# Performance work log

Hardware: AMD Instinct MI355X
Metric: run time of the kernel (lower is better)

The kernel has to match this reference:

```python
import jax, jax.numpy as jnp
import numpy as np

B, N, D, H = 32, 4096, 768, 384

def setup_inputs() -> dict:
    key = jax.random.key(0)
    k1, k2, k3 = jax.random.split(key, 3)
    patch_tokens = jax.random.normal(k1, (B, N, D), dtype=jnp.float32)
    # score head params (kaiming-like scale)
    w1 = jax.random.normal(k2, (D, H), dtype=jnp.float32) * (2.0 / H) ** 0.5
    b1 = jnp.zeros((H,), dtype=jnp.float32)
    w2 = jax.random.normal(k3, (H,), dtype=jnp.float32) * (2.0 / 1) ** 0.5
    b2 = jnp.zeros((), dtype=jnp.float32)
    return {"patch_tokens": patch_tokens, "w1": w1, "b1": b1, "w2": w2, "b2": b2,
            "keep_ratio_pct": 50}

def reference(patch_tokens, w1, b1, w2, b2, keep_ratio_pct):
    # score head: Linear -> GELU (erf variant, torch default) -> Linear(->1)
    h = jax.nn.gelu(jnp.einsum('bnd,dh->bnh', patch_tokens, w1) + b1, approximate=False)
    patch_logits = jnp.einsum('bnh,h->bn', h, w2) + b2                 # [B, N]
    foreground_scores = jax.nn.sigmoid(patch_logits)                    # [B, N]

    patch_count = patch_tokens.shape[1]
    keep_count = max(1, int(patch_count * keep_ratio_pct / 100))
    keep_count = min(keep_count, patch_count)

    if keep_count == patch_count:
        keep_mask = jnp.ones_like(foreground_scores)
    else:
        topk_scores, _ = jax.lax.top_k(foreground_scores, keep_count)   # [B, k], sorted desc
        keep_threshold = jax.lax.stop_gradient(topk_scores[:, -1:])     # [B, 1]
        keep_mask = (foreground_scores >= keep_threshold).astype(foreground_scores.dtype)

    filtered_scores = foreground_scores * keep_mask
    filtered_weights = filtered_scores / (jnp.sum(filtered_scores, axis=1, keepdims=True) + 1e-12)
    filtered_feat = jnp.einsum('bn,bnd->bd', filtered_weights, patch_tokens)  # [B, D]
    return (filtered_feat, filtered_weights, foreground_scores, keep_mask)
```

## Files before the change

kernel.cpp:

```cpp
#include <hip/hip_runtime.h>
#include <math.h>

#define BB 32
#define NN 4096
#define DD 768
#define HH 384
#define NCH 8

typedef _Float16 half8 __attribute__((ext_vector_type(8)));
typedef float f32x4 __attribute__((ext_vector_type(4)));

__global__ __launch_bounds__(64) void fapf_prep_w(
    const float* __restrict__ w1, short* __restrict__ whf, short* __restrict__ wlf)
{
    const int cf = blockIdx.x;
    const int kg = blockIdx.y;
    const int l  = threadIdx.x;
    const int c  = cf * 16 + (l & 15);
    const int kb = kg * 32 + (l >> 4) * 8;

    short hs[8], ls[8];
#pragma unroll
    for (int i = 0; i < 8; i++) {
        float v = w1[(size_t)(kb + i) * HH + c];
        _Float16 hi = (_Float16)v;
        _Float16 lo = (_Float16)(v - (float)hi);
        hs[i] = *(short*)&hi;
        ls[i] = *(short*)&lo;
    }
    size_t base = ((size_t)(kg * 24 + cf) * 64 + l) * 8;
#pragma unroll
    for (int i = 0; i < 8; i++) { whf[base + i] = hs[i]; wlf[base + i] = ls[i]; }
}

__global__ __launch_bounds__(256)
__attribute__((amdgpu_waves_per_eu(3)))
void fapf_scores_mfma(
    const float* __restrict__ x, const short* __restrict__ whf,
    const short* __restrict__ wlf, const float* __restrict__ b1,
    const float* __restrict__ w2, const float* __restrict__ b2,
    float* __restrict__ scores)
{
    __shared__ __align__(16) short xh[2][32 * 64];
    __shared__ __align__(16) short xl[2][32 * 64];
    __shared__ float part[32][4];

    const int tid = threadIdx.x;
    const int l   = tid & 63;
    const int cw  = tid >> 6;
    const int t0  = blockIdx.x * 32;

    f32x4 acc[2][6];
#pragma unroll
    for (int fr = 0; fr < 2; fr++)
#pragma unroll
        for (int cf = 0; cf < 6; cf++) acc[fr][cf] = (f32x4){0.f, 0.f, 0.f, 0.f};

    const half8* whp = (const half8*)whf + (size_t)(cw * 6) * 64 + l;
    const half8* wlp = (const half8*)wlf + (size_t)(cw * 6) * 64 + l;

    float4 xv[2];

#define LOADX(ch)                                                            \
    {                                                                        \
        _Pragma("unroll")                                                    \
        for (int it = 0; it < 2; it++) {                                     \
            int id = it * 256 + tid;                                         \
            xv[it] = *(const float4*)&x[(size_t)(t0 + (id >> 4)) * DD        \
                                        + (ch) * 64 + (id & 15) * 4];        \
        }                                                                    \
    }

#define SPLITWRITE(buf)                                                      \
    {                                                                        \
        _Pragma("unroll")                                                    \
        for (int it = 0; it < 2; it++) {                                     \
            int id = it * 256 + tid;                                         \
            int row = id >> 4, seg = id & 15;                                \
            union { short s[4]; uint2 u; } ph, pl;                           \
            float vv[4] = {xv[it].x, xv[it].y, xv[it].z, xv[it].w};          \
            _Pragma("unroll")                                                \
            for (int i = 0; i < 4; i++) {                                    \
                _Float16 hi = (_Float16)vv[i];                               \
                _Float16 lo = (_Float16)(vv[i] - (float)hi);                 \
                ph.s[i] = *(short*)&hi;                                      \
                pl.s[i] = *(short*)&lo;                                      \
            }                                                                \
            int idx = (row * 64 + seg * 4) ^ ((row & 7) << 3);               \
            *(uint2*)&xh[buf][idx] = ph.u;                                   \
            *(uint2*)&xl[buf][idx] = pl.u;                                   \
        }                                                                    \
    }

#define LOADB(dst, ptr, kg)                                                  \
    {                                                                        \
        _Pragma("unroll")                                                    \
        for (int cf = 0; cf < 6; cf++)                                       \
            dst[cf] = (ptr)[(size_t)(kg) * 1536 + (size_t)cf * 64];          \
    }

    LOADX(0);
    SPLITWRITE(0);
    half8 bA[6], bB[6];
    LOADB(bA, whp, 0);
    __syncthreads();

    for (int c = 0; c < 12; c++) {
        const int cur = c & 1;

#pragma unroll
        for (int ks = 0; ks < 2; ks++) {
            const int kg = c * 2 + ks;

            half8 ah[2], al[2];
#pragma unroll
            for (int fr = 0; fr < 2; fr++) {
                int row = fr * 16 + (l & 15);
                int idx = (row * 64 + ks * 32 + (l >> 4) * 8) ^ ((row & 7) << 3);
                ah[fr] = *(const half8*)&xh[cur][idx];
                al[fr] = *(const half8*)&xl[cur][idx];
            }

            LOADB(bB, wlp, kg);

            __builtin_amdgcn_s_setprio(1);
#pragma unroll
            for (int fr = 0; fr < 2; fr++)
#pragma unroll
                for (int cf = 0; cf < 6; cf++)
                    acc[fr][cf] = __builtin_amdgcn_mfma_f32_16x16x32_f16(
                        ah[fr], bA[cf], acc[fr][cf], 0, 0, 0);
#pragma unroll
            for (int fr = 0; fr < 2; fr++)
#pragma unroll
                for (int cf = 0; cf < 6; cf++)
                    acc[fr][cf] = __builtin_amdgcn_mfma_f32_16x16x32_f16(
                        al[fr], bA[cf], acc[fr][cf], 0, 0, 0);
            __builtin_amdgcn_s_setprio(0);

            if (kg < 23) LOADB(bA, whp, kg + 1);
            if (ks == 0 && c < 11) LOADX(c + 1);

            __builtin_amdgcn_s_setprio(1);
#pragma unroll
            for (int fr = 0; fr < 2; fr++)
#pragma unroll
                for (int cf = 0; cf < 6; cf++)
                    acc[fr][cf] = __builtin_amdgcn_mfma_f32_16x16x32_f16(
                        ah[fr], bB[cf], acc[fr][cf], 0, 0, 0);
            __builtin_amdgcn_s_setprio(0);
        }

        if (c < 11) {
            SPLITWRITE(cur ^ 1);
            __syncthreads();
        }
    }

    float b1v[6], w2v[6];
#pragma unroll
    for (int cf = 0; cf < 6; cf++) {
        int col = cw * 96 + cf * 16 + (l & 15);
        b1v[cf] = b1[col];
        w2v[cf] = w2[col];
    }
    float p[2][4];
#pragma unroll
    for (int fr = 0; fr < 2; fr++)
#pragma unroll
        for (int j = 0; j < 4; j++) p[fr][j] = 0.f;
#pragma unroll
    for (int fr = 0; fr < 2; fr++)
#pragma unroll
        for (int cf = 0; cf < 6; cf++)
#pragma unroll
            for (int j = 0; j < 4; j++) {
                float hh = acc[fr][cf][j] + b1v[cf];
                float g  = 0.5f * hh * (1.f + erff(hh * 0.70710678118654752f));
                p[fr][j] = fmaf(g, w2v[cf], p[fr][j]);
            }
#pragma unroll
    for (int m = 8; m >= 1; m >>= 1)
#pragma unroll
        for (int fr = 0; fr < 2; fr++)
#pragma unroll
            for (int j = 0; j < 4; j++)
                p[fr][j] += __shfl_xor(p[fr][j], m, 64);

    if ((l & 15) == 0) {
#pragma unroll
        for (int fr = 0; fr < 2; fr++)
#pragma unroll
            for (int j = 0; j < 4; j++) {
                int row = fr * 16 + (l >> 4) * 4 + j;
                part[row][cw] = p[fr][j];
            }
    }
    __syncthreads();
    if (tid < 32) {
        float lg = part[tid][0] + part[tid][1] + part[tid][2] + part[tid][3] + b2[0];
        scores[t0 + tid] = 1.f / (1.f + expf(-lg));
    }
#undef LOADX
#undef SPLITWRITE
#undef LOADB
}

__global__ __launch_bounds__(1024) void fapf_select_kernel(
    const float* __restrict__ scores, const int* __restrict__ pct_p,
    float* __restrict__ weights, float* __restrict__ mask,
    float* __restrict__ feat, int* __restrict__ kidx,
    float* __restrict__ kw, int* __restrict__ kcnt)
{
    __shared__ float s[NN];
    __shared__ unsigned int hist[256];
    __shared__ unsigned int sh_bin, sh_above;
    __shared__ float wsum[16];
    __shared__ int scnt;
    const int b = blockIdx.x, tid = threadIdx.x;

    if (tid == 0) scnt = 0;
    for (int i = tid; i < DD; i += 1024) feat[b * DD + i] = 0.f;
    for (int i = tid; i < NN; i += 1024) s[i] = scores[b * NN + i];

    int pct = pct_p[0];
    long long kcl = (long long)NN * pct / 100;
    int kc = (int)kcl;
    if (kc < 1) kc = 1;
    if (kc > NN) kc = NN;

    __syncthreads();

    unsigned int prefix = 0;
    unsigned int kk = (unsigned int)kc;
#pragma unroll
    for (int pass = 0; pass < 4; pass++) {
        const int shift = 24 - pass * 8;
        if (tid < 256) hist[tid] = 0;
        __syncthreads();
        const unsigned int maskAbove =
            (pass == 0) ? 0u : (0xFFFFFFFFu << (shift + 8));
        for (int i = tid; i < NN; i += 1024) {
            unsigned int u = __float_as_uint(s[i]);
            if ((u & maskAbove) == prefix)
                atomicAdd(&hist[(u >> shift) & 0xFFu], 1u);
        }
        __syncthreads();
        if (tid < 64) {
            const int ln = tid;
            unsigned int h0 = hist[4 * ln + 0], h1 = hist[4 * ln + 1];
            unsigned int h2 = hist[4 * ln + 2], h3 = hist[4 * ln + 3];
            unsigned int lsum = h0 + h1 + h2 + h3;
            unsigned int incl = lsum;
#pragma unroll
            for (int off = 1; off < 64; off <<= 1) {
                unsigned int t = __shfl_down(incl, off, 64);
                if (ln + off < 64) incl += t;
            }
            unsigned int above_lanes = incl - lsum;
            unsigned int c3 = above_lanes + h3;
            unsigned int c2 = c3 + h2;
            unsigned int c1 = c2 + h1;
            unsigned int c0 = c1 + h0;
            if (c3 >= kk && above_lanes < kk) { sh_bin = 4u * ln + 3u; sh_above = above_lanes; }
            if (c2 >= kk && c3 < kk)          { sh_bin = 4u * ln + 2u; sh_above = c3; }
            if (c1 >= kk && c2 < kk)          { sh_bin = 4u * ln + 1u; sh_above = c2; }
            if (c0 >= kk && c1 < kk)          { sh_bin = 4u * ln + 0u; sh_above = c1; }
        }
        __syncthreads();
        kk -= sh_above;
        prefix |= (sh_bin << shift);
    }
    const float thr = __uint_as_float(prefix);

    float local = 0.f;
    for (int i = tid; i < NN; i += 1024) {
        float v = s[i];
        if (v >= thr) local += v;
    }
#pragma unroll
    for (int off = 32; off >= 1; off >>= 1) local += __shfl_down(local, off, 64);
    if ((tid & 63) == 0) wsum[tid >> 6] = local;
    __syncthreads();
    if (tid < 64) {
        float t = (tid < 16) ? wsum[tid] : 0.f;
#pragma unroll
        for (int off = 8; off >= 1; off >>= 1) t += __shfl_down(t, off, 64);
        if (tid == 0) wsum[0] = t;
    }
    __syncthreads();
    const float inv = 1.f / (wsum[0] + 1e-12f);

    const int lane = tid & 63;
    for (int i = tid; i < NN; i += 1024) {
        float v = s[i];
        bool keep = (v >= thr);
        float m = keep ? 1.f : 0.f;
        weights[b * NN + i] = v * m * inv;
        mask[b * NN + i]    = m;
        if (kidx) {
            unsigned long long bal = __ballot(keep);
            int base = 0;
            if (lane == 0) base = atomicAdd(&scnt, __popcll(bal));
            base = __shfl(base, 0, 64);
            if (keep) {
                int off = __popcll(bal & ((1ULL << lane) - 1ULL));
                kidx[b * NN + base + off] = i;
                kw[b * NN + base + off]   = v * inv;
            }
        }
    }
    if (kidx) {
        __syncthreads();
        if (tid == 0) kcnt[b] = scnt;
    }
}

__global__ __launch_bounds__(256) void fapf_feat_compact(
    const float* __restrict__ x, const int* __restrict__ kidx,
    const float* __restrict__ kw, const int* __restrict__ kcnt,
    float* __restrict__ feat)
{
    const int b  = blockIdx.y;
    const int d0 = blockIdx.x * 256;
    const int ch = blockIdx.z;
    const int dl = threadIdx.x & 63;
    const int ng = threadIdx.x >> 6;

    const int cnt = kcnt[b];
    int per = (cnt + NCH - 1) / NCH;
    int j0 = ch * per; if (j0 > cnt) j0 = cnt;
    int j1 = j0 + per; if (j1 > cnt) j1 = cnt;
    int len = j1 - j0;
    int per_w = (len + 3) >> 2;
    int s = j0 + ng * per_w;
    int e = s + per_w; if (e > j1) e = j1;

    const float* xb  = x + (size_t)b * NN * DD + d0 + dl * 4;
    const int*   ib  = kidx + b * NN;
    const float* wbp = kw + b * NN;

    float4 a[8];
#pragma unroll
    for (int u = 0; u < 8; u++) a[u] = (float4){0.f, 0.f, 0.f, 0.f};

    int j = s;
    for (; j + 8 <= e; j += 8) {
        int   idx[8];
        float ww[8];
#pragma unroll
        for (int u = 0; u < 8; u++) { idx[u] = ib[j + u]; ww[u] = wbp[j + u]; }
        float4 v[8];
#pragma unroll
        for (int u = 0; u < 8; u++)
            v[u] = *(const float4*)&xb[(size_t)idx[u] * DD];
#pragma unroll
        for (int u = 0; u < 8; u++) {
            a[u].x = fmaf(ww[u], v[u].x, a[u].x);
            a[u].y = fmaf(ww[u], v[u].y, a[u].y);
            a[u].z = fmaf(ww[u], v[u].z, a[u].z);
            a[u].w = fmaf(ww[u], v[u].w, a[u].w);
        }
    }
    for (; j < e; j++) {
        float w = wbp[j];
        float4 v = *(const float4*)&xb[(size_t)ib[j] * DD];
        a[0].x = fmaf(w, v.x, a[0].x);
        a[0].y = fmaf(w, v.y, a[0].y);
        a[0].z = fmaf(w, v.z, a[0].z);
        a[0].w = fmaf(w, v.w, a[0].w);
    }

    float4 acc;
    acc.x = ((a[0].x + a[1].x) + (a[2].x + a[3].x)) + ((a[4].x + a[5].x) + (a[6].x + a[7].x));
    acc.y = ((a[0].y + a[1].y) + (a[2].y + a[3].y)) + ((a[4].y + a[5].y) + (a[6].y + a[7].y));
    acc.z = ((a[0].z + a[1].z) + (a[2].z + a[3].z)) + ((a[4].z + a[5].z) + (a[6].z + a[7].z));
    acc.w = ((a[0].w + a[1].w) + (a[2].w + a[3].w)) + ((a[4].w + a[5].w) + (a[6].w + a[7].w));

    __shared__ float4 red[4][64];
    red[ng][dl] = acc;
    __syncthreads();
    if (threadIdx.x < 64) {
        float4 r0 = red[0][dl], r1 = red[1][dl], r2 = red[2][dl], r3 = red[3][dl];
        float* fp = &feat[b * DD + d0 + dl * 4];
        atomicAdd(&fp[0], (r0.x + r1.x) + (r2.x + r3.x));
        atomicAdd(&fp[1], (r0.y + r1.y) + (r2.y + r3.y));
        atomicAdd(&fp[2], (r0.z + r1.z) + (r2.z + r3.z));
        atomicAdd(&fp[3], (r0.w + r1.w) + (r2.w + r3.w));
    }
}

__global__ __launch_bounds__(256) void fapf_feat_dense(
    const float* __restrict__ x, const float* __restrict__ weights,
    float* __restrict__ feat)
{
    const int b  = blockIdx.y;
    const int d0 = blockIdx.x * 64;
    const int dl = threadIdx.x & 63;
    const int ng = threadIdx.x >> 6;

    const float* xb = x + (size_t)b * NN * DD;
    const float* wb = weights + b * NN;

    float a0 = 0.f, a1 = 0.f, a2 = 0.f, a3 = 0.f;
    for (int n = ng; n < NN; n += 16) {
        float w0 = wb[n], w1v = wb[n + 4], w2v = wb[n + 8], w3 = wb[n + 12];
        float v0 = xb[(size_t)(n)      * DD + d0 + dl];
        float v1 = xb[(size_t)(n + 4)  * DD + d0 + dl];
        float v2 = xb[(size_t)(n + 8)  * DD + d0 + dl];
        float v3 = xb[(size_t)(n + 12) * DD + d0 + dl];
        a0 = fmaf(w0, v0, a0);
        a1 = fmaf(w1v, v1, a1);
        a2 = fmaf(w2v, v2, a2);
        a3 = fmaf(w3, v3, a3);
    }
    float acc = (a0 + a1) + (a2 + a3);

    __shared__ float red[4][64];
    red[ng][dl] = acc;
    __syncthreads();
    if (threadIdx.x < 64) {
        feat[b * DD + d0 + dl] =
            (red[0][dl] + red[1][dl]) + (red[2][dl] + red[3][dl]);
    }
}

extern "C" void kernel_launch(void* const* d_in, const int* in_sizes, int n_in,
                              void* d_out, int out_size, void* d_ws, size_t ws_size,
                              hipStream_t stream) {
    const float* x   = (const float*)d_in[0];
    const float* w1  = (const float*)d_in[1];
    const float* b1  = (const float*)d_in[2];
    const float* w2  = (const float*)d_in[3];
    const float* b2  = (const float*)d_in[4];
    const int*   pct = (const int*)d_in[5];

    float* out = (float*)d_out;
    float* feat    = out;
    float* weights = out + BB * DD;
    float* scores  = weights + BB * NN;
    float* mask    = scores + BB * NN;

    short* whf  = (short*)d_ws;
    short* wlf  = whf + 24 * 24 * 64 * 8;
    int*   kidx = (int*)(wlf + 24 * 24 * 64 * 8);
    float* kw   = (float*)(kidx + BB * NN);
    int*   kcnt = (int*)(kw + BB * NN);

    const size_t needed = 2 * (size_t)(24 * 24 * 64 * 8) * sizeof(short)
                        + (size_t)BB * NN * (sizeof(int) + sizeof(float))
                        + BB * sizeof(int);
    const bool compact = ws_size >= needed;

    fapf_prep_w<<<dim3(24, 24), dim3(64), 0, stream>>>(w1, whf, wlf);
    fapf_scores_mfma<<<dim3(BB * NN / 32), dim3(256), 0, stream>>>(
        x, whf, wlf, b1, w2, b2, scores);
    fapf_select_kernel<<<dim3(BB), dim3(1024), 0, stream>>>(
        scores, pct, weights, mask, feat,
        compact ? kidx : (int*)nullptr, kw, kcnt);
    if (compact) {
        fapf_feat_compact<<<dim3(DD / 256, BB, NCH), dim3(256), 0, stream>>>(
            x, kidx, kw, kcnt, feat);
    } else {
        fapf_feat_dense<<<dim3(DD / 64, BB), dim3(256), 0, stream>>>(
            x, weights, feat);
    }
}
```

Measured before the change: 305.6 us.

## Load x fragments directly into registers, drop LDS staging and barriers

```diff
diff --git a/kernel.cpp b/kernel.cpp
--- a/kernel.cpp
+++ b/kernel.cpp
@@ -41,8 +41,6 @@
     const float* __restrict__ w2, const float* __restrict__ b2,
     float* __restrict__ scores)
 {
-    __shared__ __align__(16) short xh[2][32 * 64];
-    __shared__ __align__(16) short xl[2][32 * 64];
     __shared__ float part[32][4];
 
     const int tid = threadIdx.x;
@@ -59,38 +57,8 @@
     const half8* whp = (const half8*)whf + (size_t)(cw * 6) * 64 + l;
     const half8* wlp = (const half8*)wlf + (size_t)(cw * 6) * 64 + l;
 
-    float4 xv[2];
-
-#define LOADX(ch)                                                            \
-    {                                                                        \
-        _Pragma("unroll")                                                    \
-        for (int it = 0; it < 2; it++) {                                     \
-            int id = it * 256 + tid;                                         \
-            xv[it] = *(const float4*)&x[(size_t)(t0 + (id >> 4)) * DD        \
-                                        + (ch) * 64 + (id & 15) * 4];        \
-        }                                                                    \
-    }
-
-#define SPLITWRITE(buf)                                                      \
-    {                                                                        \
-        _Pragma("unroll")                                                    \
-        for (int it = 0; it < 2; it++) {                                     \
-            int id = it * 256 + tid;                                         \
-            int row = id >> 4, seg = id & 15;                                \
-            union { short s[4]; uint2 u; } ph, pl;                           \
-            float vv[4] = {xv[it].x, xv[it].y, xv[it].z, xv[it].w};          \
-            _Pragma("unroll")                                                \
-            for (int i = 0; i < 4; i++) {                                    \
-                _Float16 hi = (_Float16)vv[i];                               \
-                _Float16 lo = (_Float16)(vv[i] - (float)hi);                 \
-                ph.s[i] = *(short*)&hi;                                      \
-                pl.s[i] = *(short*)&lo;                                      \
-            }                                                                \
-            int idx = (row * 64 + seg * 4) ^ ((row & 7) << 3);               \
-            *(uint2*)&xh[buf][idx] = ph.u;                                   \
-            *(uint2*)&xl[buf][idx] = pl.u;                                   \
-        }                                                                    \
-    }
+    const float* xr0 = x + (size_t)(t0 + (l & 15)) * DD + (l >> 4) * 8;
+    const float* xr1 = xr0 + (size_t)16 * DD;
 
 #define LOADB(dst, ptr, kg)                                                  \
     {                                                                        \
@@ -99,62 +67,74 @@
             dst[cf] = (ptr)[(size_t)(kg) * 1536 + (size_t)cf * 64];          \
     }
 
-    LOADX(0);
-    SPLITWRITE(0);
     half8 bA[6], bB[6];
+    float4 xv[4];
+
     LOADB(bA, whp, 0);
-    __syncthreads();
-
-    for (int c = 0; c < 12; c++) {
-        const int cur = c & 1;
-
-#pragma unroll
-        for (int ks = 0; ks < 2; ks++) {
-            const int kg = c * 2 + ks;
-
-            half8 ah[2], al[2];
-#pragma unroll
-            for (int fr = 0; fr < 2; fr++) {
-                int row = fr * 16 + (l & 15);
-                int idx = (row * 64 + ks * 32 + (l >> 4) * 8) ^ ((row & 7) << 3);
-                ah[fr] = *(const half8*)&xh[cur][idx];
-                al[fr] = *(const half8*)&xl[cur][idx];
+    xv[0] = *(const float4*)(xr0);
+    xv[1] = *(const float4*)(xr0 + 4);
+    xv[2] = *(const float4*)(xr1);
+    xv[3] = *(const float4*)(xr1 + 4);
+
+    for (int kg = 0; kg < 24; kg++) {
+        LOADB(bB, wlp, kg);
+
+        half8 ah[2], al[2];
+        {
+            union { short s[8]; half8 h; } uh0, ul0, uh1, ul1;
+            float f0[8] = {xv[0].x, xv[0].y, xv[0].z, xv[0].w,
+                           xv[1].x, xv[1].y, xv[1].z, xv[1].w};
+            float f1[8] = {xv[2].x, xv[2].y, xv[2].z, xv[2].w,
+                           xv[3].x, xv[3].y, xv[3].z, xv[3].w};
+#pragma unroll
+            for (int i = 0; i < 8; i++) {
+                _Float16 h0 = (_Float16)f0[i];
+                _Float16 g0 = (_Float16)(f0[i] - (float)h0);
+                uh0.s[i] = *(short*)&h0;
+                ul0.s[i] = *(short*)&g0;
+                _Float16 h1 = (_Float16)f1[i];
+                _Float16 g1 = (_Float16)(f1[i] - (float)h1);
+                uh1.s[i] = *(short*)&h1;
+                ul1.s[i] = *(short*)&g1;
             }
-
-            LOADB(bB, wlp, kg);
-
-            __builtin_amdgcn_s_setprio(1);
-#pragma unroll
-            for (int fr = 0; fr < 2; fr++)
-#pragma unroll
-                for (int cf = 0; cf < 6; cf++)
-                    acc[fr][cf] = __builtin_amdgcn_mfma_f32_16x16x32_f16(
-                        ah[fr], bA[cf], acc[fr][cf], 0, 0, 0);
-#pragma unroll
-            for (int fr = 0; fr < 2; fr++)
-#pragma unroll
-                for (int cf = 0; cf < 6; cf++)
-                    acc[fr][cf] = __builtin_amdgcn_mfma_f32_16x16x32_f16(
-                        al[fr], bA[cf], acc[fr][cf], 0, 0, 0);
-            __builtin_amdgcn_s_setprio(0);
-
-            if (kg < 23) LOADB(bA, whp, kg + 1);
-            if (ks == 0 && c < 11) LOADX(c + 1);
-
-            __builtin_amdgcn_s_setprio(1);
-#pragma unroll
-            for (int fr = 0; fr < 2; fr++)
-#pragma unroll
-                for (int cf = 0; cf < 6; cf++)
-                    acc[fr][cf] = __builtin_amdgcn_mfma_f32_16x16x32_f16(
-                        ah[fr], bB[cf], acc[fr][cf], 0, 0, 0);
-            __builtin_amdgcn_s_setprio(0);
-        }
-
-        if (c < 11) {
-            SPLITWRITE(cur ^ 1);
-            __syncthreads();
-        }
+            ah[0] = uh0.h; al[0] = ul0.h;
+            ah[1] = uh1.h; al[1] = ul1.h;
+        }
+
+        if (kg < 23) {
+            const float* p0 = xr0 + (size_t)(kg + 1) * 32;
+            const float* p1 = xr1 + (size_t)(kg + 1) * 32;
+            xv[0] = *(const float4*)(p0);
+            xv[1] = *(const float4*)(p0 + 4);
+            xv[2] = *(const float4*)(p1);
+            xv[3] = *(const float4*)(p1 + 4);
+        }
+
+        __builtin_amdgcn_s_setprio(1);
+#pragma unroll
+        for (int fr = 0; fr < 2; fr++)
+#pragma unroll
+            for (int cf = 0; cf < 6; cf++)
+                acc[fr][cf] = __builtin_amdgcn_mfma_f32_16x16x32_f16(
+                    ah[fr], bA[cf], acc[fr][cf], 0, 0, 0);
+#pragma unroll
+        for (int fr = 0; fr < 2; fr++)
+#pragma unroll
+            for (int cf = 0; cf < 6; cf++)
+                acc[fr][cf] = __builtin_amdgcn_mfma_f32_16x16x32_f16(
+                    al[fr], bA[cf], acc[fr][cf], 0, 0, 0);
+        __builtin_amdgcn_s_setprio(0);
+
+        if (kg < 23) LOADB(bA, whp, kg + 1);
+
+        __builtin_amdgcn_s_setprio(1);
+#pragma unroll
+        for (int fr = 0; fr < 2; fr++)
+#pragma unroll
+            for (int cf = 0; cf < 6; cf++)
+                acc[fr][cf] = __builtin_amdgcn_mfma_f32_16x16x32_f16(
+                    ah[fr], bB[cf], acc[fr][cf], 0, 0, 0);
+        __builtin_amdgcn_s_setprio(0);
     }
 
     float b1v[6], w2v[6];
@@ -201,8 +181,6 @@
         float lg = part[tid][0] + part[tid][1] + part[tid][2] + part[tid][3] + b2[0];
         scores[t0 + tid] = 1.f / (1.f + expf(-lg));
     }
-#undef LOADX
-#undef SPLITWRITE
 #undef LOADB
 }
 
```

Result: slower. 431.0 us (+41.0%).
